# Optimization experiments

Measured on AMD Instinct MI355X. Metric: run time of the kernel, lower is better.

## Reference

```python
import jax, jax.numpy as jnp
import numpy as np

N, IN_DIM, OUT_DIM, HEADS, SUB = 4096, 256, 128, 4, 32
ETA = 0.5
LAMBDA_SPARSE = 0.05
NEG_BIG = -1e9


def setup_inputs() -> dict:
    key = jax.random.key(0)
    k1, k2, k3, k4 = jax.random.split(key, 4)
    H = jax.random.normal(k1, (N, IN_DIM), dtype=jnp.float32)
    # sparse binary adjacency mask (avg degree ~ 41) with self-loops
    adj_mask = (jax.random.uniform(k2, (N, N)) < 0.01).astype(jnp.float32)
    adj_mask = adj_mask.at[jnp.arange(N), jnp.arange(N)].set(1.0)
    # per-head orthonormal subspace bases U_k = QR(randn)[:, :SUB]
    raw = jax.random.normal(k3, (HEADS, IN_DIM, SUB), dtype=jnp.float32)
    U = jax.vmap(lambda r: jnp.linalg.qr(r)[0])(raw)  # [h, D, s]
    threshold = jnp.full((OUT_DIM,), LAMBDA_SPARSE, dtype=jnp.float32)
    proj_w = jax.random.normal(k4, (OUT_DIM, IN_DIM), dtype=jnp.float32) / np.float32(np.sqrt(IN_DIM))
    return {"H": H, "adj_mask": adj_mask, "U": U, "threshold": threshold, "proj_w": proj_w}


def reference(H, adj_mask, U, threshold, proj_w):
    # Z_k = U_k^T @ H^T  -> [h, s, N]
    Z = jnp.einsum('hds,nd->hsn', U, H)
    # scores_k = Z_k^T @ Z_k / sqrt(s)  -> [h, N, N]
    scores = jnp.einsum('hsn,hsm->hnm', Z, Z) / jnp.sqrt(jnp.float32(SUB))
    scores = scores + (1.0 - adj_mask)[None, :, :] * NEG_BIG
    alpha = jax.nn.softmax(scores, axis=-1)  # torch softmax(dim=1) on [N,N] rows
    # agg_k = Z_k @ alpha_k^T  -> [h, s, N];  sum_k U_k @ agg_k -> [D, N]
    agg = jnp.einsum('hsj,hij->hsi', Z, alpha)
    agg_sum = jnp.einsum('hds,hsn->dn', U, agg)
    H_half = H + ETA * agg_sum.T           # [N, D]
    H_half = H_half @ proj_w.T             # [N, out_dim]
    # soft-threshold
    H_out = jnp.sign(H_half) * jax.nn.relu(jnp.abs(H_half) - threshold[None, :])
    # orthogonality loss: sum_k ||U_k^T U_k - I||_F^2 + sum_{k<l} ||U_k^T U_l||_F^2
    G = jnp.einsum('kds,ldt->klst', U, U)  # [h, h, s, s]
    eye_s = jnp.eye(SUB, dtype=U.dtype)
    eye_h = jnp.eye(HEADS, dtype=U.dtype)
    sub = G - eye_h[:, :, None, None] * eye_s[None, None, :, :]
    sq = jnp.sum(sub ** 2, axis=(2, 3))    # [h, h]
    orth_loss = jnp.sum(jnp.triu(jnp.ones((HEADS, HEADS), dtype=U.dtype)) * sq)
    return H_out, orth_loss
```

## Files before the change

### kernel.cpp

```cpp
#include <hip/hip_runtime.h>
#include <hip/hip_bf16.h>
#include <math.h>

#define NN 4096
#define IN_DIM 256
#define OUT_DIM 128
#define HEADS 4
#define SUB 32
#define MAXDEG 128
#define ETA 0.5f
#define INV_SQRT_SUB 0.17677669529663687f

__global__ __launch_bounds__(256) void fused_small(const float* __restrict__ U,
                                                   const float* __restrict__ PW,
                                                   float* __restrict__ Wcomb,
                                                   float* __restrict__ W2,
                                                   float* __restrict__ loss) {
    int b = blockIdx.x;
    int t = threadIdx.x;
    __shared__ float sh[260];

    if (b < 256) {
        float v;
        if (b < 128) {
            int h = b >> 5, s = b & 31;
            v = U[h * IN_DIM * SUB + t * SUB + s];
        } else {
            v = PW[(b - 128) * IN_DIM + t];
        }
        Wcomb[b * IN_DIM + t] = v;
    } else if (b < 384) {
        int hs = b - 256;
        int h = hs >> 5, s = hs & 31;
        sh[t] = U[h * IN_DIM * SUB + t * SUB + s];
        __syncthreads();
        if (t < 128) {
            const float4* pw4 = (const float4*)(PW + t * IN_DIM);
            const float4* u4  = (const float4*)sh;
            float acc = 0.f;
            #pragma unroll 4
            for (int d4 = 0; d4 < 64; ++d4) {
                float4 a = u4[d4], p = pw4[d4];
                acc += a.x * p.x + a.y * p.y + a.z * p.z + a.w * p.w;
            }
            W2[hs * OUT_DIM + t] = acc;
        }
    } else {
        const int pk[10] = {0,0,0,0,1,1,1,2,2,3};
        const int pl[10] = {0,1,2,3,1,2,3,2,3,3};
        int p = b - 384;
        int k = pk[p], l = pl[p];
        int t2 = t & 31;
        int sg = t >> 5;
        const float* Uk = U + k * IN_DIM * SUB;
        const float* Ul = U + l * IN_DIM * SUB;
        float a0 = 0.f, a1 = 0.f, a2 = 0.f, a3 = 0.f;
        #pragma unroll 4
        for (int d = 0; d < IN_DIM; ++d) {
            float ul = Ul[d * SUB + t2];
            float u0 = Uk[d * SUB + sg * 4 + 0];
            float u1 = Uk[d * SUB + sg * 4 + 1];
            float u2 = Uk[d * SUB + sg * 4 + 2];
            float u3 = Uk[d * SUB + sg * 4 + 3];
            a0 += u0 * ul; a1 += u1 * ul; a2 += u2 * ul; a3 += u3 * ul;
        }
        if (k == l) {
            if (sg * 4 + 0 == t2) a0 -= 1.f;
            if (sg * 4 + 1 == t2) a1 -= 1.f;
            if (sg * 4 + 2 == t2) a2 -= 1.f;
            if (sg * 4 + 3 == t2) a3 -= 1.f;
        }
        float local = a0 * a0 + a1 * a1 + a2 * a2 + a3 * a3;
        local += __shfl_xor(local, 32, 64);
        local += __shfl_xor(local, 16, 64);
        local += __shfl_xor(local, 8, 64);
        local += __shfl_xor(local, 4, 64);
        local += __shfl_xor(local, 2, 64);
        local += __shfl_xor(local, 1, 64);
        if ((t & 63) == 0) sh[256 + (t >> 6)] = local;
        __syncthreads();
        if (t == 0) atomicAdd(loss, sh[256] + sh[257] + sh[258] + sh[259]);
    }
}

#define RPB 4
__global__ __launch_bounds__(256) void compute_zt_p(const float* __restrict__ H,
                                                    const float* __restrict__ Wcomb,
                                                    float* __restrict__ ZT,
                                                    float* __restrict__ P) {
    int t = threadIdx.x;
    int r0 = blockIdx.x * RPB;
    __shared__ float Hs[RPB][IN_DIM];
    const float4* H4 = (const float4*)(H + (size_t)r0 * IN_DIM);
    ((float4*)&Hs[0][0])[t] = H4[t];
    __syncthreads();

    float acc[RPB];
    #pragma unroll
    for (int r = 0; r < RPB; ++r) acc[r] = 0.f;

    const float4* Wr = (const float4*)(Wcomb + t * IN_DIM);
    float4 w0 = Wr[0], w1 = Wr[1];
    #pragma unroll 4
    for (int d4 = 0; d4 < 64; ++d4) {
        float4 wn = Wr[(d4 + 2 < 64) ? d4 + 2 : 63];
        float4 w = w0; w0 = w1; w1 = wn;
        #pragma unroll
        for (int r = 0; r < RPB; ++r) {
            float4 h = *(const float4*)&Hs[r][d4 * 4];
            acc[r] += h.x * w.x + h.y * w.y + h.z * w.z + h.w * w.w;
        }
    }
    #pragma unroll
    for (int r = 0; r < RPB; ++r) {
        if (t < 128) ZT[(size_t)(r0 + r) * 128 + t] = acc[r];
        else         P [(size_t)(r0 + r) * 128 + (t - 128)] = acc[r];
    }
}

__global__ __launch_bounds__(128) void attn_core(const float* __restrict__ ZT,
                                                 const float* __restrict__ adj,
                                                 float* __restrict__ agg) {
    int i = blockIdx.x;
    int t = threadIdx.x;
    __shared__ int   nbr_s[MAXDEG];
    __shared__ float e_s[MAXDEG][HEADS];
    __shared__ float z_s[128];
    __shared__ int cnt;

    const float4* row4 = (const float4*)(adj + (size_t)i * NN);
    float4 v[8];
    #pragma unroll
    for (int k = 0; k < 8; ++k) v[k] = row4[t + k * 128];

    if (t == 0) cnt = 0;
    nbr_s[t] = 0;
    z_s[t] = ZT[(size_t)i * 128 + t];
    __syncthreads();

    #pragma unroll
    for (int k = 0; k < 8; ++k) {
        int j0 = (t + k * 128) * 4;
        if (v[k].x > 0.5f) { int p = atomicAdd(&cnt, 1); if (p < MAXDEG) nbr_s[p] = j0; }
        if (v[k].y > 0.5f) { int p = atomicAdd(&cnt, 1); if (p < MAXDEG) nbr_s[p] = j0 + 1; }
        if (v[k].z > 0.5f) { int p = atomicAdd(&cnt, 1); if (p < MAXDEG) nbr_s[p] = j0 + 2; }
        if (v[k].w > 0.5f) { int p = atomicAdd(&cnt, 1); if (p < MAXDEG) nbr_s[p] = j0 + 3; }
    }
    __syncthreads();
    int dg = cnt < MAXDEG ? cnt : MAXDEG;

    int jj0 = t >> 2, h = t & 3;
    int ntiles = (dg + 31) >> 5;
    const float4* qr = (const float4*)(&z_s[h * 32]);
    for (int tile = 0; tile < ntiles; ++tile) {
        int jj = tile * 32 + jj0;
        int j = nbr_s[jj];
        const float4* zr = (const float4*)(ZT + (size_t)j * 128 + h * 32);
        float acc = 0.f;
        #pragma unroll
        for (int k = 0; k < 8; ++k) {
            float4 z = zr[k];
            float4 q = qr[k];
            acc += z.x * q.x + z.y * q.y + z.z * q.z + z.w * q.w;
        }
        e_s[jj][h] = (jj < dg) ? __expf(acc * INV_SQRT_SUB) : 0.f;
    }
    __syncthreads();

    int hh = t >> 5;
    float accV = 0.f, accS = 0.f;
    const float* zbase = ZT + t;
    for (int jj = 0; jj < dg; jj += 4) {
        int ja = nbr_s[jj],     jb = nbr_s[jj + 1];
        int jc = nbr_s[jj + 2], jd = nbr_s[jj + 3];
        float ea = e_s[jj][hh],     eb = e_s[jj + 1][hh];
        float ec = e_s[jj + 2][hh], ed = e_s[jj + 3][hh];
        float va = zbase[(size_t)ja * 128], vb = zbase[(size_t)jb * 128];
        float vc = zbase[(size_t)jc * 128], vd = zbase[(size_t)jd * 128];
        accV += ea * va + eb * vb + ec * vc + ed * vd;
        accS += (ea + eb) + (ec + ed);
    }
    agg[(size_t)i * 128 + t] = accV * (ETA / accS);
}

#define EROWS 16
__global__ __launch_bounds__(256) void epilogue(const float* __restrict__ Pm,
                                                const float* __restrict__ agg,
                                                const float* __restrict__ W2,
                                                const float* __restrict__ threshold,
                                                float* __restrict__ out) {
    int t = threadIdx.x;
    int o = t & 127, half = t >> 7;
    int r0 = blockIdx.x * EROWS;
    __shared__ float As[EROWS][128];
    const float4* a4 = (const float4*)(agg + (size_t)r0 * 128);
    float4* As4 = (float4*)&As[0][0];
    As4[t]       = a4[t];
    As4[t + 256] = a4[t + 256];
    __syncthreads();

    float acc[8];
    #pragma unroll
    for (int r = 0; r < 8; ++r) acc[r] = 0.f;

    for (int q4 = 0; q4 < 32; ++q4) {
        int hs = q4 * 4;
        float w0 = W2[(hs + 0) * 128 + o];
        float w1 = W2[(hs + 1) * 128 + o];
        float w2v = W2[(hs + 2) * 128 + o];
        float w3 = W2[(hs + 3) * 128 + o];
        #pragma unroll
        for (int r = 0; r < 8; ++r) {
            float4 a = *(const float4*)&As[half * 8 + r][hs];
            acc[r] += a.x * w0 + a.y * w1 + a.z * w2v + a.w * w3;
        }
    }
    float th = threshold[o];
    #pragma unroll
    for (int r = 0; r < 8; ++r) {
        int row = r0 + half * 8 + r;
        float val = Pm[(size_t)row * 128 + o] + acc[r];
        float av = fabsf(val) - th;
        out[(size_t)row * 128 + o] = (av > 0.f) ? copysignf(av, val) : 0.f;
    }
}

extern "C" void kernel_launch(void* const* d_in, const int* in_sizes, int n_in,
                              void* d_out, int out_size, void* d_ws, size_t ws_size,
                              hipStream_t stream) {
    const float* H   = (const float*)d_in[0];
    const float* adj = (const float*)d_in[1];
    const float* U   = (const float*)d_in[2];
    const float* thr = (const float*)d_in[3];
    const float* PW  = (const float*)d_in[4];
    float* out = (float*)d_out;
    float* loss = out + (size_t)NN * OUT_DIM;

    char* ws = (char*)d_ws;
    float* ZT    = (float*)(ws);
    float* P     = (float*)(ws + (size_t)2097152);
    float* agg   = (float*)(ws + (size_t)4194304);
    float* W2    = (float*)(ws + (size_t)6291456);
    float* Wcomb = (float*)(ws + (size_t)6356992);

    hipMemsetAsync(loss, 0, sizeof(float), stream);
    fused_small<<<394, 256, 0, stream>>>(U, PW, Wcomb, W2, loss);
    compute_zt_p<<<NN / RPB, 256, 0, stream>>>(H, Wcomb, ZT, P);
    attn_core<<<NN, 128, 0, stream>>>(ZT, adj, agg);
    epilogue<<<NN / EROWS, 256, 0, stream>>>(P, agg, W2, thr, out);
}
```

Measured before the change: 176.2 us.

## Use split-bf16 MFMA for Z/P projection and drop loss memset

Replaces the scalar FP32 projection kernel with a matrix-core kernel that splits H and the combined weights into bf16 hi/lo parts and runs three MFMA passes to approximate FP32 accuracy. It also replaces the memset plus atomicAdd for the orthogonality loss with per-block partial sums that the epilogue adds up, which removes one launch. The projection was ALU-bound at about 0.27 GFLOP. In exchange it does extra conversion work and carries some precision risk from the three-term bf16 split.

```diff
diff --git a/kernel.cpp b/kernel.cpp
--- a/kernel.cpp
+++ b/kernel.cpp
@@ -11,11 +11,26 @@
 #define ETA 0.5f
 #define INV_SQRT_SUB 0.17677669529663687f
 
+typedef __attribute__((ext_vector_type(8))) short bf16x8;
+typedef __attribute__((ext_vector_type(4))) short s16x4;
+typedef __attribute__((ext_vector_type(4))) float f32x4;
+
+static __device__ inline short f2bf(float f) {
+    unsigned u = __float_as_uint(f);
+    unsigned r = u + 0x7FFFu + ((u >> 16) & 1u);
+    return (short)(r >> 16);
+}
+static __device__ inline float bf2f(short s) {
+    return __uint_as_float(((unsigned)(unsigned short)s) << 16);
+}
+#define MFMA16(a, b, c) __builtin_amdgcn_mfma_f32_16x16x32_bf16(a, b, c, 0, 0, 0)
+
 __global__ __launch_bounds__(256) void fused_small(const float* __restrict__ U,
                                                    const float* __restrict__ PW,
-                                                   float* __restrict__ Wcomb,
+                                                   short* __restrict__ Wh,
+                                                   short* __restrict__ Wl,
                                                    float* __restrict__ W2,
-                                                   float* __restrict__ loss) {
+                                                   float* __restrict__ loss_parts) {
     int b = blockIdx.x;
     int t = threadIdx.x;
     __shared__ float sh[260];
@@ -28,7 +43,9 @@
         } else {
             v = PW[(b - 128) * IN_DIM + t];
         }
-        Wcomb[b * IN_DIM + t] = v;
+        short hi = f2bf(v);
+        Wh[b * IN_DIM + t] = hi;
+        Wl[b * IN_DIM + t] = f2bf(v - bf2f(hi));
     } else if (b < 384) {
         int hs = b - 256;
         int h = hs >> 5, s = hs & 31;
@@ -79,42 +96,79 @@
         local += __shfl_xor(local, 1, 64);
         if ((t & 63) == 0) sh[256 + (t >> 6)] = local;
         __syncthreads();
-        if (t == 0) atomicAdd(loss, sh[256] + sh[257] + sh[258] + sh[259]);
-    }
-}
-
-#define RPB 4
-__global__ __launch_bounds__(256) void compute_zt_p(const float* __restrict__ H,
-                                                    const float* __restrict__ Wcomb,
-                                                    float* __restrict__ ZT,
-                                                    float* __restrict__ P) {
-    int t = threadIdx.x;
-    int r0 = blockIdx.x * RPB;
-    __shared__ float Hs[RPB][IN_DIM];
-    const float4* H4 = (const float4*)(H + (size_t)r0 * IN_DIM);
-    ((float4*)&Hs[0][0])[t] = H4[t];
-    __syncthreads();
-
-    float acc[RPB];
-    #pragma unroll
-    for (int r = 0; r < RPB; ++r) acc[r] = 0.f;
-
-    const float4* Wr = (const float4*)(Wcomb + t * IN_DIM);
-    float4 w0 = Wr[0], w1 = Wr[1];
-    #pragma unroll 4
-    for (int d4 = 0; d4 < 64; ++d4) {
-        float4 wn = Wr[(d4 + 2 < 64) ? d4 + 2 : 63];
-        float4 w = w0; w0 = w1; w1 = wn;
+        if (t == 0) loss_parts[p] = sh[256] + sh[257] + sh[258] + sh[259];
+    }
+}
+
+#define LDA 264
+__global__ __launch_bounds__(256) void ztp_mfma(const float* __restrict__ H,
+                                                const short* __restrict__ Wh,
+                                                const short* __restrict__ Wl,
+                                                float* __restrict__ ZT,
+                                                float* __restrict__ P) {
+    __shared__ short Ah[16 * LDA];
+    __shared__ short Al[16 * LDA];
+    int t = threadIdx.x, b = blockIdx.x;
+    int m0 = (b >> 1) * 16, chalf = b & 1;
+
+    {
+        int r = t >> 4, dbase = (t & 15) * 16;
+        const float4* src = (const float4*)(H + (size_t)(m0 + r) * IN_DIM + dbase);
         #pragma unroll
-        for (int r = 0; r < RPB; ++r) {
-            float4 h = *(const float4*)&Hs[r][d4 * 4];
-            acc[r] += h.x * w.x + h.y * w.y + h.z * w.z + h.w * w.w;
-        }
-    }
-    #pragma unroll
-    for (int r = 0; r < RPB; ++r) {
-        if (t < 128) ZT[(size_t)(r0 + r) * 128 + t] = acc[r];
-        else         P [(size_t)(r0 + r) * 128 + (t - 128)] = acc[r];
+        for (int q = 0; q < 4; ++q) {
+            float4 f = src[q];
+            float fv[4] = {f.x, f.y, f.z, f.w};
+            s16x4 hi, lo;
+            #pragma unroll
+            for (int j = 0; j < 4; ++j) {
+                short h = f2bf(fv[j]);
+                hi[j] = h;
+                lo[j] = f2bf(fv[j] - bf2f(h));
+            }
+            *(s16x4*)&Ah[r * LDA + dbase + q * 4] = hi;
+            *(s16x4*)&Al[r * LDA + dbase + q * 4] = lo;
+        }
+    }
+    __syncthreads();
+
+    int wave = t >> 6, lane = t & 63;
+    int c0 = chalf * 128 + wave * 32;
+    int arow = lane & 15, agrp = lane >> 4;
+
+    const short* ahp = &Ah[arow * LDA + agrp * 8];
+    const short* alp = &Al[arow * LDA + agrp * 8];
+    const short* bh0 = Wh + (size_t)(c0 + arow) * IN_DIM + agrp * 8;
+    const short* bl0 = Wl + (size_t)(c0 + arow) * IN_DIM + agrp * 8;
+    const short* bh1 = bh0 + 16 * IN_DIM;
+    const short* bl1 = bl0 + 16 * IN_DIM;
+
+    f32x4 acc0 = {0.f, 0.f, 0.f, 0.f};
+    f32x4 acc1 = {0.f, 0.f, 0.f, 0.f};
+
+    #pragma unroll
+    for (int kk = 0; kk < 8; ++kk) {
+        int d0 = kk * 32;
+        bf16x8 a_h = *(const bf16x8*)(ahp + d0);
+        bf16x8 a_l = *(const bf16x8*)(alp + d0);
+        bf16x8 b0h = *(const bf16x8*)(bh0 + d0);
+        bf16x8 b0l = *(const bf16x8*)(bl0 + d0);
+        bf16x8 b1h = *(const bf16x8*)(bh1 + d0);
+        bf16x8 b1l = *(const bf16x8*)(bl1 + d0);
+        acc0 = MFMA16(a_h, b0h, acc0);
+        acc0 = MFMA16(a_h, b0l, acc0);
+        acc0 = MFMA16(a_l, b0h, acc0);
+        acc1 = MFMA16(a_h, b1h, acc1);
+        acc1 = MFMA16(a_h, b1l, acc1);
+        acc1 = MFMA16(a_l, b1h, acc1);
+    }
+
+    float* dst = chalf ? P : ZT;
+    int colbase = c0 - chalf * 128;
+    #pragma unroll
+    for (int i = 0; i < 4; ++i) {
+        int row = m0 + agrp * 4 + i;
+        dst[(size_t)row * 128 + colbase + arow]      = acc0[i];
+        dst[(size_t)row * 128 + colbase + 16 + arow] = acc1[i];
     }
 }
 
@@ -188,6 +242,7 @@
                                                 const float* __restrict__ agg,
                                                 const float* __restrict__ W2,
                                                 const float* __restrict__ threshold,
+                                                const float* __restrict__ loss_parts,
                                                 float* __restrict__ out) {
     int t = threadIdx.x;
     int o = t & 127, half = t >> 7;
@@ -197,6 +252,13 @@
     float4* As4 = (float4*)&As[0][0];
     As4[t]       = a4[t];
     As4[t + 256] = a4[t + 256];
+
+    if (blockIdx.x == 0 && t == 0) {
+        float L = 0.f;
+        #pragma unroll
+        for (int p = 0; p < 10; ++p) L += loss_parts[p];
+        out[(size_t)NN * OUT_DIM] = L;
+    }
     __syncthreads();
 
     float acc[8];
@@ -234,18 +296,18 @@
     const float* thr = (const float*)d_in[3];
     const float* PW  = (const float*)d_in[4];
     float* out = (float*)d_out;
-    float* loss = out + (size_t)NN * OUT_DIM;
 
     char* ws = (char*)d_ws;
     float* ZT    = (float*)(ws);
     float* P     = (float*)(ws + (size_t)2097152);
     float* agg   = (float*)(ws + (size_t)4194304);
     float* W2    = (float*)(ws + (size_t)6291456);
-    float* Wcomb = (float*)(ws + (size_t)6356992);
-
-    hipMemsetAsync(loss, 0, sizeof(float), stream);
-    fused_small<<<394, 256, 0, stream>>>(U, PW, Wcomb, W2, loss);
-    compute_zt_p<<<NN / RPB, 256, 0, stream>>>(H, Wcomb, ZT, P);
+    short* Wh    = (short*)(ws + (size_t)6356992);
+    short* Wl    = (short*)(ws + (size_t)6488064);
+    float* lossp = (float*)(ws + (size_t)6619136);
+
+    fused_small<<<394, 256, 0, stream>>>(U, PW, Wh, Wl, W2, lossp);
+    ztp_mfma<<<NN / 16 * 2, 256, 0, stream>>>(H, Wh, Wl, ZT, P);
     attn_core<<<NN, 128, 0, stream>>>(ZT, adj, agg);
-    epilogue<<<NN / EROWS, 256, 0, stream>>>(P, agg, W2, thr, out);
-}
+    epilogue<<<NN / EROWS, 256, 0, stream>>>(P, agg, W2, thr, lossp, out);
+}
```

New measurement: 151.7 us. 1.16x faster.
